# Kernel tuning notes

Measured on AMD Instinct MI355X. Metric: run time of the kernel, lower is better.

Reference implementation:

```python
import jax, jax.numpy as jnp
import numpy as np


def _consts():
    # Hypercube vertices: itertools.product([-1,1], repeat=n) order => MSB-first bits.
    def verts(nbits):
        idx = np.arange(2 ** nbits)
        return (((idx[:, None] >> np.arange(nbits - 1, -1, -1)[None, :]) & 1) * 2.0 - 1.0).astype(np.float32)

    hexagrams = verts(6)   # (64, 6)
    q2_verts = verts(2)    # (4, 2)
    q3_verts = verts(3)    # (8, 3)

    # Q2 vertex -> group one-hot, _Q2_TO_GROUP = [2, 1, 1, 0]
    q2_to_group = np.zeros((4, 3), dtype=np.float32)
    for v, g in enumerate([2, 1, 1, 0]):
        q2_to_group[v, g] = 1.0

    # Group anchors: ABSTRACT = mean(hex[63], hex[62]), DYNAMIC = mean(hex[19], hex[21]),
    # CONCRETE = mean(hex[0], hex[8]); then L2-normalized.
    anch = np.stack([
        hexagrams[[63, 62]].mean(0),
        hexagrams[[19, 21]].mean(0),
        hexagrams[[0, 8]].mean(0),
    ]).astype(np.float32)
    anch = anch / np.clip(np.linalg.norm(anch, axis=-1, keepdims=True), 1e-12, None)

    # Walsh-Hadamard popcount masks, pre-divided by their sums -> (64, 3) matrix.
    bits = np.array([bin(i).count('1') for i in range(64)], dtype=np.float32)
    wa = (bits >= 5).astype(np.float32)
    wd = (bits == 3).astype(np.float32)
    wc = (bits <= 1).astype(np.float32)
    wht_mat = np.stack([wa / wa.sum(), wd / wd.sum(), wc / wc.sum()], axis=1)

    return tuple(jnp.asarray(a) for a in (hexagrams, q2_verts, q3_verts, q2_to_group, anch, wht_mat))


def _q3_to_group_init():
    q3_map = np.zeros((8, 3), dtype=np.float32)
    for i in range(8):
        yc = bin(i).count('1')
        if yc == 0:
            q3_map[i, 2] = 1.0
        elif yc == 1:
            q3_map[i, 1] = 1.0
        elif yc == 2:
            q3_map[i, 0] = 0.6
            q3_map[i, 1] = 0.4
        else:
            q3_map[i, 0] = 1.0
    q3_map = q3_map / np.clip(q3_map.sum(axis=1, keepdims=True), 1e-8, None)
    return q3_map


def setup_inputs() -> dict:
    key = jax.random.key(0)
    k_x, k2, k3, k6 = jax.random.split(key, 4)
    B, T, D = 4, 4096, 2048
    s = 1.0 / float(np.sqrt(D))  # torch Linear default init range
    return {
        'x': jax.random.normal(k_x, (B, T, D), dtype=jnp.float32),
        'ln_w': jnp.ones((D,), dtype=jnp.float32),
        'ln_b': jnp.zeros((D,), dtype=jnp.float32),
        'w_q2': jax.random.uniform(k2, (2, D), minval=-s, maxval=s, dtype=jnp.float32),
        'w_q3': jax.random.uniform(k3, (3, D), minval=-s, maxval=s, dtype=jnp.float32),
        'w_q6': jax.random.uniform(k6, (6, D), minval=-s, maxval=s, dtype=jnp.float32),
        'log_temp': jnp.asarray(np.log(0.5), dtype=jnp.float32),
        'log_scale_mix': jnp.zeros((3,), dtype=jnp.float32),
        'q3_to_group': jnp.asarray(_q3_to_group_init()),
        'log_wht_mix': jnp.asarray(-2.0, dtype=jnp.float32),
    }


def _forward(x, ln_w, ln_b, w_q2, w_q3, w_q6, log_temp, log_scale_mix, q3_to_group, log_wht_mix):
    hexa, q2v, q3v, q2g, anch, wht_mat = _consts()

    # LayerNorm (eps = 1e-5, torch default)
    mu = x.mean(-1, keepdims=True)
    var = ((x - mu) ** 2).mean(-1, keepdims=True)
    h = (x - mu) * jax.lax.rsqrt(var + 1e-5) * ln_w + ln_b

    temp = jnp.clip(jnp.exp(log_temp), 0.1, 5.0)

    # Q2 scale: (B,T,2) -> 4 vertices -> 3 groups
    w2 = jax.nn.softmax(jnp.tanh(h @ w_q2.T) @ q2v.T / temp, axis=-1)
    score_q2 = w2 @ q2g

    # Q3 scale: (B,T,3) -> 8 vertices -> learned soft group map
    w3 = jax.nn.softmax(jnp.tanh(h @ w_q3.T) @ q3v.T / temp, axis=-1)
    score_q3 = w3 @ jax.nn.softmax(q3_to_group, axis=-1)

    # Q6 scale: (B,T,6) -> 64 hexagram vertices
    hex_w = jax.nn.softmax(jnp.tanh(h @ w_q6.T) @ hexa.T / temp, axis=-1)
    score_cos = (hex_w @ hexa) @ anch.T            # cosine-sim vs normalized anchors
    score_wht = hex_w @ wht_mat                    # popcount-mask averages
    alpha = jax.nn.sigmoid(log_wht_mix)
    score_q6 = (1.0 - alpha) * score_cos + alpha * score_wht

    mix = jax.nn.softmax(log_scale_mix)
    group_w = jax.nn.softmax(mix[0] * score_q2 + mix[1] * score_q3 + mix[2] * score_q6, axis=-1)

    mg = group_w.mean(axis=(0, 1))
    mh = hex_w.mean(axis=(0, 1))
    lb_loss = jnp.sum(mg * jnp.log(mg + 1e-8)) + 0.1 * jnp.sum(mh * jnp.log(mh + 1e-8))
    return group_w, hex_w, lb_loss


def reference(x, ln_w, ln_b, w_q2, w_q3, w_q6, log_temp, log_scale_mix, q3_to_group, log_wht_mix):
    return _forward(x, ln_w, ln_b, w_q2, w_q3, w_q6, log_temp, log_scale_mix, q3_to_group, log_wht_mix)
```

## Files before the change

### kernel.cpp

```cpp
#include <hip/hip_runtime.h>
#include <math.h>
#include <string.h>

#define D 2048
#define NTOK 16384
#define NROW 11
#define MROWS_U32 (NROW * D / 2)
#define K1_BLOCKS 1024
#define K1_THREADS 256
#define WSTRIDE_U 1036
#define TILE_S 20

#define WS_A 0
#define WS_B 16
#define WS_IT 32
#define WS_ALPHA 33
#define WS_MIX 34
#define WS_M3 40
#define WS_MERGED 64
#define WS_PART (WS_MERGED + MROWS_U32)

typedef __fp16 h2 __attribute__((ext_vector_type(2)));
typedef __fp16 h8 __attribute__((ext_vector_type(8)));
typedef float f32x4 __attribute__((ext_vector_type(4)));

__device__ __forceinline__ float wsum(float v){
#pragma unroll
  for (int m = 1; m < 64; m <<= 1) v += __shfl_xor(v, m, 64);
  return v;
}
__device__ __forceinline__ float wmax(float v){
#pragma unroll
  for (int m = 1; m < 64; m <<= 1) v = fmaxf(v, __shfl_xor(v, m, 64));
  return v;
}
__device__ __forceinline__ float rcp_fast(float x){ return __builtin_amdgcn_rcpf(x); }
__device__ __forceinline__ float tanh_fast(float x){
  float e = __expf(2.0f * x);
  return 1.0f - 2.0f * rcp_fast(e + 1.0f);
}
__device__ __forceinline__ float sload(const float* __restrict__ p){
  return __uint_as_float(__builtin_amdgcn_readfirstlane(__float_as_uint(*p)));
}
__device__ __forceinline__ unsigned int h2u(h2 h){ unsigned int u; memcpy(&u, &h, 4); return u; }

__global__ __launch_bounds__(256) void k0_prep(
    const float* __restrict__ ln_w, const float* __restrict__ ln_b,
    const float* __restrict__ w_q2, const float* __restrict__ w_q3,
    const float* __restrict__ w_q6,
    const float* __restrict__ log_temp, const float* __restrict__ log_scale_mix,
    const float* __restrict__ q3_to_group, const float* __restrict__ log_wht_mix,
    float* __restrict__ ws)
{
  const int tid = threadIdx.x;
  const int k = blockIdx.x;
  unsigned int* wsu = (unsigned int*)ws;
  if (k < NROW){
    const float* row = (k < 2) ? (w_q2 + (size_t)k * D)
                     : (k < 5) ? (w_q3 + (size_t)(k - 2) * D)
                               : (w_q6 + (size_t)(k - 5) * D);
    float pa = 0.f, pb = 0.f;
    for (int i = tid * 2; i < D; i += 512){
      float w0 = row[i], w1 = row[i + 1];
      h2 h = __builtin_amdgcn_cvt_pkrtz(ln_w[i] * w0, ln_w[i + 1] * w1);
      pa += (float)h[0] + (float)h[1];
      pb = fmaf(ln_b[i], w0, pb);
      pb = fmaf(ln_b[i + 1], w1, pb);
      wsu[WS_MERGED + k * 1024 + i / 2] = h2u(h);
    }
    __shared__ float red[8];
    pa = wsum(pa); pb = wsum(pb);
    if ((tid & 63) == 0){ red[tid >> 6] = pa; red[4 + (tid >> 6)] = pb; }
    __syncthreads();
    if (tid == 0){
      ws[WS_A + k] = red[0] + red[1] + red[2] + red[3];
      ws[WS_B + k] = red[4] + red[5] + red[6] + red[7];
    }
  } else if (tid == 0){
    float t = __expf(log_temp[0]);
    t = fminf(fmaxf(t, 0.1f), 5.0f);
    ws[WS_IT] = 1.0f / t;
    ws[WS_ALPHA] = 1.0f / (1.0f + __expf(-log_wht_mix[0]));
    float m0 = log_scale_mix[0], m1 = log_scale_mix[1], m2 = log_scale_mix[2];
    float mm = fmaxf(m0, fmaxf(m1, m2));
    float e0 = __expf(m0 - mm), e1 = __expf(m1 - mm), e2 = __expf(m2 - mm);
    float inv = 1.0f / (e0 + e1 + e2);
    ws[WS_MIX + 0] = e0 * inv; ws[WS_MIX + 1] = e1 * inv; ws[WS_MIX + 2] = e2 * inv;
    for (int r = 0; r < 8; ++r){
      float v0 = q3_to_group[r*3+0], v1 = q3_to_group[r*3+1], v2 = q3_to_group[r*3+2];
      float mx = fmaxf(v0, fmaxf(v1, v2));
      float f0 = __expf(v0 - mx), f1 = __expf(v1 - mx), f2 = __expf(v2 - mx);
      float iv = 1.0f / (f0 + f1 + f2);
      ws[WS_M3 + r*3 + 0] = f0 * iv;
      ws[WS_M3 + r*3 + 1] = f1 * iv;
      ws[WS_M3 + r*3 + 2] = f2 * iv;
    }
  }
}

__global__ __launch_bounds__(256) void k1_main(
    const float* __restrict__ x, const float* __restrict__ ws,
    float* __restrict__ gout, float* __restrict__ hout, float* __restrict__ part)
{
  __shared__ unsigned int sW[NROW * WSTRIDE_U];
  __shared__ float tile[4][16][TILE_S];
  __shared__ float lred[4][68];
  const int tid  = threadIdx.x;
  const int lane = tid & 63;
  const int wid  = tid >> 6;
  const int blk  = blockIdx.x;
  const int tok0 = blk * 16;
  const int n = lane & 15;
  const int q = lane >> 4;

  const float* xp = x + (size_t)(tok0 + n) * D + wid * 512 + q * 8;

  float4 xa[16];
#pragma unroll
  for (int s = 0; s < 8; ++s){
    xa[2*s]     = *(const float4*)(xp + s * 32);
    xa[2*s + 1] = *(const float4*)(xp + s * 32 + 4);
  }

  {
    const uint4* src = (const uint4*)((const unsigned int*)ws + WS_MERGED);
#pragma unroll
    for (int j = 0; j < 11; ++j){
      int idx = tid + j * 256;
      int r = idx >> 8, i = idx & 255;
      *(uint4*)(sW + r * WSTRIDE_U + i * 4) = src[r * 256 + i];
    }
  }

  float sq = 0.f;
  h8 hxA[8], hxB[8];
#pragma unroll
  for (int s = 0; s < 8; ++s){
    float4 f0 = xa[2*s], f1 = xa[2*s + 1];
    sq = fmaf(f0.x,f0.x, fmaf(f0.y,f0.y, fmaf(f0.z,f0.z, fmaf(f0.w,f0.w, sq))));
    sq = fmaf(f1.x,f1.x, fmaf(f1.y,f1.y, fmaf(f1.z,f1.z, fmaf(f1.w,f1.w, sq))));
    h2 p0 = __builtin_amdgcn_cvt_pkrtz(f0.x, f0.y);
    h2 p1 = __builtin_amdgcn_cvt_pkrtz(f0.z, f0.w);
    h2 p2 = __builtin_amdgcn_cvt_pkrtz(f1.x, f1.y);
    h2 p3 = __builtin_amdgcn_cvt_pkrtz(f1.z, f1.w);
    h8 A;
    A[0]=p0[0]; A[1]=p0[1]; A[2]=p1[0]; A[3]=p1[1];
    A[4]=p2[0]; A[5]=p2[1]; A[6]=p3[0]; A[7]=p3[1];
    hxA[s] = A;
  }
#pragma unroll
  for (int s = 0; s < 8; ++s){
    xa[2*s]     = *(const float4*)(xp + (s + 8) * 32);
    xa[2*s + 1] = *(const float4*)(xp + (s + 8) * 32 + 4);
  }

  __syncthreads();

  const int wr = (n < NROW) ? n : (n - NROW);
  const bool is_ones = (n == NROW);
  const uint4 ones4 = make_uint4(0x3C003C00u, 0x3C003C00u, 0x3C003C00u, 0x3C003C00u);
  const unsigned int* wb = sW + wr * WSTRIDE_U + wid * 256 + q * 4;

  f32x4 acc = {0.f, 0.f, 0.f, 0.f};

#pragma unroll
  for (int s = 0; s < 8; ++s){
    uint4 wq = *(const uint4*)(wb + s * 16);
    if (is_ones) wq = ones4;
    h8 B; memcpy(&B, &wq, 16);
    acc = __builtin_amdgcn_mfma_f32_16x16x32_f16(hxA[s], B, acc, 0, 0, 0);
  }

#pragma unroll
  for (int s = 0; s < 8; ++s){
    float4 f0 = xa[2*s], f1 = xa[2*s + 1];
    sq = fmaf(f0.x,f0.x, fmaf(f0.y,f0.y, fmaf(f0.z,f0.z, fmaf(f0.w,f0.w, sq))));
    sq = fmaf(f1.x,f1.x, fmaf(f1.y,f1.y, fmaf(f1.z,f1.z, fmaf(f1.w,f1.w, sq))));
    h2 p0 = __builtin_amdgcn_cvt_pkrtz(f0.x, f0.y);
    h2 p1 = __builtin_amdgcn_cvt_pkrtz(f0.z, f0.w);
    h2 p2 = __builtin_amdgcn_cvt_pkrtz(f1.x, f1.y);
    h2 p3 = __builtin_amdgcn_cvt_pkrtz(f1.z, f1.w);
    h8 A;
    A[0]=p0[0]; A[1]=p0[1]; A[2]=p1[0]; A[3]=p1[1];
    A[4]=p2[0]; A[5]=p2[1]; A[6]=p3[0]; A[7]=p3[1];
    hxB[s] = A;
  }

#pragma unroll
  for (int s = 0; s < 8; ++s){
    uint4 wq = *(const uint4*)(wb + (s + 8) * 16);
    if (is_ones) wq = ones4;
    h8 B; memcpy(&B, &wq, 16);
    acc = __builtin_amdgcn_mfma_f32_16x16x32_f16(hxB[s], B, acc, 0, 0, 0);
  }

  sq += __shfl_xor(sq, 16, 64);
  sq += __shfl_xor(sq, 32, 64);

#pragma unroll
  for (int r = 0; r < 4; ++r) tile[wid][q * 4 + r][n] = acc[r];
  if (lane < 16) tile[wid][lane][16] = sq;

  __syncthreads();

  float a[NROW], bb[NROW];
#pragma unroll
  for (int k = 0; k < NROW; ++k){ a[k] = sload(ws + WS_A + k); bb[k] = sload(ws + WS_B + k); }
  const float it    = sload(ws + WS_IT);
  const float alpha = sload(ws + WS_ALPHA);
  const float mix0 = sload(ws + WS_MIX), mix1 = sload(ws + WS_MIX + 1), mix2 = sload(ws + WS_MIX + 2);
  float M3r[8][3];
#pragma unroll
  for (int r = 0; r < 8; ++r){
#pragma unroll
    for (int g = 0; g < 3; ++g) M3r[r][g] = sload(ws + WS_M3 + r*3 + g);
  }

  float sgn[6];
#pragma unroll
  for (int j = 0; j < 6; ++j) sgn[j] = ((lane >> (5 - j)) & 1) ? 1.0f : -1.0f;
  const float C5 = 0.44721359549995793f;
  const float A0c[6] = { C5,  C5,  C5,  C5,  C5, 0.f };
  const float A1c[6] = {-0.5f, 0.5f, -0.5f, 0.f, 0.f, 0.5f};
  const float A2c[6] = {-C5, -C5, 0.f, -C5, -C5, -C5};
  float cs0 = 0.f, cs1 = 0.f, cs2 = 0.f;
#pragma unroll
  for (int j = 0; j < 6; ++j){
    cs0 = fmaf(sgn[j], A0c[j], cs0);
    cs1 = fmaf(sgn[j], A1c[j], cs1);
    cs2 = fmaf(sgn[j], A2c[j], cs2);
  }
  const int pc = __popc(lane);
  const float w7c = 1.0f / 7.0f;
  float wh0 = (pc >= 5) ? w7c  : 0.f;
  float wh1 = (pc == 3) ? 0.05f: 0.f;
  float wh2 = (pc <= 1) ? w7c  : 0.f;
  const float m60 = (1.f - alpha)*cs0 + alpha*wh0;
  const float m61 = (1.f - alpha)*cs1 + alpha*wh1;
  const float m62 = (1.f - alpha)*cs2 + alpha*wh2;

  float hsum = 0.f, ga0 = 0.f, ga1 = 0.f, ga2 = 0.f;

#pragma unroll 1
  for (int i = 0; i < 4; ++i){
    const int tl  = wid * 4 + i;
    const int tok = tok0 + tl;

    float t[12]; float sqv = 0.f;
#pragma unroll
    for (int k = 0; k < 12; ++k) t[k] = 0.f;
#pragma unroll
    for (int hh = 0; hh < 4; ++hh){
      const float* row = &tile[hh][tl][0];
      float4 c0 = *(const float4*)(row);
      float4 c1 = *(const float4*)(row + 4);
      float4 c2 = *(const float4*)(row + 8);
      t[0] += c0.x; t[1] += c0.y; t[2]  += c0.z; t[3]  += c0.w;
      t[4] += c1.x; t[5] += c1.y; t[6]  += c1.z; t[7]  += c1.w;
      t[8] += c2.x; t[9] += c2.y; t[10] += c2.z; t[11] += c2.w;
      sqv += row[16];
    }

    float mean = t[11] * (1.0f / D);
    float var  = fmaf(sqv, 1.0f / D, -mean * mean);
    float rr   = rsqrtf(var + 1e-5f);
    float u[NROW];
#pragma unroll
    for (int k = 0; k < NROW; ++k){
      float d = fmaf(-mean, a[k], t[k]);
      u[k] = tanh_fast(fmaf(rr, d, bb[k]));
    }

    float p01 = u[0] + u[1], m01 = u[0] - u[1];
    float l0 = -p01*it, l1 = -m01*it, l2 = m01*it, l3 = p01*it;
    float mx2 = fmaxf(fmaxf(l0, l1), fmaxf(l2, l3));
    float e0 = __expf(l0-mx2), e1 = __expf(l1-mx2), e2 = __expf(l2-mx2), e3 = __expf(l3-mx2);
    float i2 = rcp_fast(e0 + e1 + e2 + e3);
    float s2g0 = e3 * i2, s2g1 = (e1 + e2) * i2, s2g2 = e0 * i2;

    float l3v[8]; float mx3 = -1e30f;
#pragma unroll
    for (int v = 0; v < 8; ++v){
      float acc3 = ((v & 4) ? u[2] : -u[2]) + ((v & 2) ? u[3] : -u[3]) + ((v & 1) ? u[4] : -u[4]);
      l3v[v] = acc3 * it;
      mx3 = fmaxf(mx3, l3v[v]);
    }
    float w3v[8]; float se3 = 0.f;
#pragma unroll
    for (int v = 0; v < 8; ++v){ w3v[v] = __expf(l3v[v] - mx3); se3 += w3v[v]; }
    float i3 = rcp_fast(se3);
    float s3g0 = 0.f, s3g1 = 0.f, s3g2 = 0.f;
#pragma unroll
    for (int v = 0; v < 8; ++v){
      s3g0 = fmaf(w3v[v], M3r[v][0], s3g0);
      s3g1 = fmaf(w3v[v], M3r[v][1], s3g1);
      s3g2 = fmaf(w3v[v], M3r[v][2], s3g2);
    }
    s3g0 *= i3; s3g1 *= i3; s3g2 *= i3;

    float lg = 0.f;
#pragma unroll
    for (int jj = 0; jj < 6; ++jj) lg = fmaf(sgn[jj], u[5 + jj], lg);
    lg *= it;
    float mx6 = wmax(lg);
    float p   = __expf(lg - mx6);
    float se6 = wsum(p);
    float hw  = p * rcp_fast(se6);
    hout[(size_t)tok * 64 + lane] = hw;
    hsum += hw;
    float s6g0 = wsum(hw * m60);
    float s6g1 = wsum(hw * m61);
    float s6g2 = wsum(hw * m62);

    float g0 = mix0*s2g0 + mix1*s3g0 + mix2*s6g0;
    float g1 = mix0*s2g1 + mix1*s3g1 + mix2*s6g1;
    float g2 = mix0*s2g2 + mix1*s3g2 + mix2*s6g2;
    float gm = fmaxf(g0, fmaxf(g1, g2));
    float y0 = __expf(g0-gm), y1 = __expf(g1-gm), y2 = __expf(g2-gm);
    float gi = rcp_fast(y0 + y1 + y2);
    float gw0 = y0*gi, gw1 = y1*gi, gw2 = y2*gi;
    ga0 += gw0; ga1 += gw1; ga2 += gw2;
    if (lane < 3){
      float val = (lane == 0) ? gw0 : (lane == 1) ? gw1 : gw2;
      gout[(size_t)tok * 3 + lane] = val;
    }
  }

  lred[wid][lane] = hsum;
  if (lane < 3){
    float val = (lane == 0) ? ga0 : (lane == 1) ? ga1 : ga2;
    lred[wid][64 + lane] = val;
  }
  __syncthreads();
  if (tid < 67){
    float v = lred[0][tid] + lred[1][tid] + lred[2][tid] + lred[3][tid];
    part[(size_t)tid * K1_BLOCKS + blk] = v;
  }
}

__global__ __launch_bounds__(1024) void k2_loss(const float* __restrict__ part,
                                                float* __restrict__ lout)
{
  __shared__ float sums[68];
  const int tid = threadIdx.x;
  const int lane = tid & 63;
  const int wid  = tid >> 6;
  for (int jv = wid; jv < 67; jv += 16){
    const float4* p = (const float4*)(part + (size_t)jv * K1_BLOCKS);
    float v = 0.f;
#pragma unroll
    for (int b = 0; b < K1_BLOCKS / 256; ++b){
      float4 q = p[lane + b * 64];
      v += (q.x + q.y) + (q.z + q.w);
    }
    v = wsum(v);
    if (lane == 0) sums[jv] = v;
  }
  __syncthreads();
  if (wid == 0){
    const float inv = 1.0f / (float)NTOK;
    float mh = sums[lane] * inv;
    float term = 0.1f * mh * logf(mh + 1e-8f);
    if (lane < 3){
      float mg = sums[64 + lane] * inv;
      term += mg * logf(mg + 1e-8f);
    }
    float L = wsum(term);
    if (lane == 0) lout[0] = L;
  }
}

extern "C" void kernel_launch(void* const* d_in, const int* in_sizes, int n_in,
                              void* d_out, int out_size, void* d_ws, size_t ws_size,
                              hipStream_t stream)
{
  const float* x             = (const float*)d_in[0];
  const float* ln_w          = (const float*)d_in[1];
  const float* ln_b          = (const float*)d_in[2];
  const float* w_q2          = (const float*)d_in[3];
  const float* w_q3          = (const float*)d_in[4];
  const float* w_q6          = (const float*)d_in[5];
  const float* log_temp      = (const float*)d_in[6];
  const float* log_scale_mix = (const float*)d_in[7];
  const float* q3_to_group   = (const float*)d_in[8];
  const float* log_wht_mix   = (const float*)d_in[9];

  float* out  = (float*)d_out;
  float* gout = out;
  float* hout = out + (size_t)NTOK * 3;
  float* lout = out + (size_t)NTOK * 3 + (size_t)NTOK * 64;
  float* ws   = (float*)d_ws;

  k0_prep<<<12, 256, 0, stream>>>(ln_w, ln_b, w_q2, w_q3, w_q6,
                                  log_temp, log_scale_mix, q3_to_group, log_wht_mix, ws);
  k1_main<<<K1_BLOCKS, K1_THREADS, 0, stream>>>(x, ws, gout, hout, ws + WS_PART);
  k2_loss<<<1, 1024, 0, stream>>>(ws + WS_PART, lout);
}
```

Before: 50.00 us.

## Parallelize scalar setup across a wavefront, move barrier, unroll token loop

Replaces the single-thread setup in the prep kernel (temperature, mix softmax and the 8-row q3 group softmax) with a 64-lane wavefront version that uses shuffles, so each output is computed by its own lane. In the main kernel, the __syncthreads is moved ahead of the second batch of x loads. The per-token epilogue loop is also fully unrolled. The setup change shortens a serial tail in a tiny kernel. Moving the barrier could change how well the x loads overlap, and unrolling raises register pressure.

```diff
diff --git a/kernel.cpp b/kernel.cpp
--- a/kernel.cpp
+++ b/kernel.cpp
@@ -76,24 +76,35 @@
       ws[WS_A + k] = red[0] + red[1] + red[2] + red[3];
       ws[WS_B + k] = red[4] + red[5] + red[6] + red[7];
     }
-  } else if (tid == 0){
-    float t = __expf(log_temp[0]);
-    t = fminf(fmaxf(t, 0.1f), 5.0f);
-    ws[WS_IT] = 1.0f / t;
-    ws[WS_ALPHA] = 1.0f / (1.0f + __expf(-log_wht_mix[0]));
-    float m0 = log_scale_mix[0], m1 = log_scale_mix[1], m2 = log_scale_mix[2];
-    float mm = fmaxf(m0, fmaxf(m1, m2));
-    float e0 = __expf(m0 - mm), e1 = __expf(m1 - mm), e2 = __expf(m2 - mm);
-    float inv = 1.0f / (e0 + e1 + e2);
-    ws[WS_MIX + 0] = e0 * inv; ws[WS_MIX + 1] = e1 * inv; ws[WS_MIX + 2] = e2 * inv;
-    for (int r = 0; r < 8; ++r){
-      float v0 = q3_to_group[r*3+0], v1 = q3_to_group[r*3+1], v2 = q3_to_group[r*3+2];
+  } else if (tid < 64){
+    const int lane = tid;
+    float q3v = (lane < 24) ? q3_to_group[lane]   : 0.f;
+    float sc  = (lane < 3)  ? log_scale_mix[lane] : 0.f;
+    float lt  = (lane == 0) ? log_temp[0]         : 0.f;
+    float lw  = (lane == 0) ? log_wht_mix[0]      : 0.f;
+
+    if (lane == 0){
+      float t = __expf(lt);
+      t = fminf(fmaxf(t, 0.1f), 5.0f);
+      ws[WS_IT] = 1.0f / t;
+      ws[WS_ALPHA] = 1.0f / (1.0f + __expf(-lw));
+    }
+    float m0 = __shfl(sc, 0, 64), m1 = __shfl(sc, 1, 64), m2 = __shfl(sc, 2, 64);
+    if (lane < 3){
+      float mm = fmaxf(m0, fmaxf(m1, m2));
+      float e0 = __expf(m0 - mm), e1 = __expf(m1 - mm), e2 = __expf(m2 - mm);
+      float inv = 1.0f / (e0 + e1 + e2);
+      ws[WS_MIX + lane] = ((lane == 0) ? e0 : (lane == 1) ? e1 : e2) * inv;
+    }
+    if (lane < 24){
+      int r = lane / 3, c = lane - r * 3;
+      float v0 = __shfl(q3v, r*3 + 0, 64);
+      float v1 = __shfl(q3v, r*3 + 1, 64);
+      float v2 = __shfl(q3v, r*3 + 2, 64);
       float mx = fmaxf(v0, fmaxf(v1, v2));
       float f0 = __expf(v0 - mx), f1 = __expf(v1 - mx), f2 = __expf(v2 - mx);
       float iv = 1.0f / (f0 + f1 + f2);
-      ws[WS_M3 + r*3 + 0] = f0 * iv;
-      ws[WS_M3 + r*3 + 1] = f1 * iv;
-      ws[WS_M3 + r*3 + 2] = f2 * iv;
+      ws[WS_M3 + lane] = ((c == 0) ? f0 : (c == 1) ? f1 : f2) * iv;
     }
   }
 }
@@ -148,13 +159,14 @@
     A[4]=p2[0]; A[5]=p2[1]; A[6]=p3[0]; A[7]=p3[1];
     hxA[s] = A;
   }
+
+  __syncthreads();
+
 #pragma unroll
   for (int s = 0; s < 8; ++s){
     xa[2*s]     = *(const float4*)(xp + (s + 8) * 32);
     xa[2*s + 1] = *(const float4*)(xp + (s + 8) * 32 + 4);
   }
-
-  __syncthreads();
 
   const int wr = (n < NROW) ? n : (n - NROW);
   const bool is_ones = (n == NROW);
@@ -241,7 +253,7 @@
 
   float hsum = 0.f, ga0 = 0.f, ga1 = 0.f, ga2 = 0.f;
 
-#pragma unroll 1
+#pragma unroll
   for (int i = 0; i < 4; ++i){
     const int tl  = wid * 4 + i;
     const int tok = tok0 + tl;
```

New measurement: 46.58 us. -6.8%, faster.
